# Performance work log

Measured on AMD Instinct MI355X. Metric: run time of the kernel, lower is better.

The kernel has to match this reference:

```python
import jax, jax.numpy as jnp
import numpy as np

N_NODES = 100000
N_EDGES = 3200000
NUM_GRAPHS = 128
IN_DIM = 15
HID = 64


def setup_inputs() -> dict:
    key = jax.random.key(0)
    ks = jax.random.split(key, 12)
    x = jax.random.normal(ks[0], (N_NODES, IN_DIM), dtype=jnp.float32)
    edge_index = jax.random.randint(ks[1], (2, N_EDGES), 0, N_NODES, dtype=jnp.int64)
    batch = jnp.sort(jax.random.randint(ks[2], (N_NODES,), 0, NUM_GRAPHS, dtype=jnp.int64))
    # Glorot-style weights for the 4 GCNConv layers, zero biases (PyG default)
    def glorot(k, fan_in, fan_out):
        s = jnp.sqrt(6.0 / (fan_in + fan_out))
        return jax.random.uniform(k, (fan_in, fan_out), jnp.float32, -s, s)
    return {
        "x": x,
        "w1": glorot(ks[3], IN_DIM, HID), "b1": jnp.zeros((HID,), jnp.float32),
        "w2": glorot(ks[4], HID, HID),    "b2": jnp.zeros((HID,), jnp.float32),
        "w3": glorot(ks[5], HID, HID),    "b3": jnp.zeros((HID,), jnp.float32),
        "w4": glorot(ks[6], HID, HID),    "b4": jnp.zeros((HID,), jnp.float32),
        "edge_index": edge_index,
        "batch": batch,
    }


def _gcn_norm(edge_index, num_nodes):
    # PyG gcn_norm with add_self_loops=True: A_hat = A + I, norm = d^-1/2[src] * d^-1/2[dst]
    loops = jnp.arange(num_nodes, dtype=edge_index.dtype)
    src = jnp.concatenate([edge_index[0], loops])
    dst = jnp.concatenate([edge_index[1], loops])
    deg = jax.ops.segment_sum(jnp.ones_like(dst, dtype=jnp.float32), dst,
                              num_segments=num_nodes)
    dis = jnp.where(deg > 0, jax.lax.rsqrt(deg), 0.0)
    norm = dis[src] * dis[dst]  # [E + N]
    return src, dst, norm


def _gcn_conv(h, w, b, src, dst, norm, num_nodes):
    h = h @ w                               # linear transform first (PyG order)
    msg = h[src] * norm[:, None]            # gather + scale  [E+N, HID]
    agg = jax.ops.segment_sum(msg, dst, num_segments=num_nodes)  # scatter-add
    return agg + b


def reference(x, w1, b1, w2, b2, w3, b3, w4, b4, edge_index, batch):
    n = x.shape[0]
    src, dst, norm = _gcn_norm(edge_index, n)
    h = jax.nn.relu(_gcn_conv(x, w1, b1, src, dst, norm, n))
    h = jax.nn.relu(_gcn_conv(h, w2, b2, src, dst, norm, n))
    h = jax.nn.relu(_gcn_conv(h, w3, b3, src, dst, norm, n))
    h = jax.nn.relu(_gcn_conv(h, w4, b4, src, dst, norm, n))
    # global_mean_pool over graph ids
    sums = jax.ops.segment_sum(h, batch, num_segments=NUM_GRAPHS)
    cnts = jax.ops.segment_sum(jnp.ones((n,), jnp.float32), batch,
                               num_segments=NUM_GRAPHS)
    return sums / jnp.maximum(cnts, 1.0)[:, None]
```

## Files before the change

kernel.cpp:

```cpp
#include <hip/hip_runtime.h>
#include <hip/hip_fp16.h>

#define NN 100000
#define NE 3200000
#define NG 128
#define HID 64

#define BSH 9
#define BNODES 512
#define NBK ((NN + BNODES - 1) / BNODES)
#define CCH 8192
#define CAP 18432

typedef __attribute__((ext_vector_type(2))) _Float16 half2v;
typedef __attribute__((ext_vector_type(4))) _Float16 half4v;

#if __has_builtin(__builtin_amdgcn_fdot2)
#define FDOT2(v, o, a) __builtin_amdgcn_fdot2((v), (o), (a), false)
#else
static __device__ inline float FDOT2(half2v v, half2v o, float a) {
    return a + (float)v.x * (float)o.x + (float)v.y * (float)o.y;
}
#endif

__global__ __launch_bounds__(256) void binit_kernel(int* __restrict__ bcur) {
    int t = threadIdx.x;
    if (t < NBK) bcur[t] = t * CAP;
}

__global__ __launch_bounds__(512) void bscatter_kernel(const int* __restrict__ src,
                                                       const int* __restrict__ dst,
                                                       int* __restrict__ bcur,
                                                       unsigned* __restrict__ pairs,
                                                       int E) {
    __shared__ unsigned stage[CCH];
    __shared__ unsigned char bb[CCH];
    __shared__ int cnt[NBK];
    __shared__ int base[NBK];
    const int e0 = blockIdx.x * CCH;
    const int n  = min(CCH, E - e0);
    if (n <= 0) return;
    for (int i = threadIdx.x; i < NBK; i += 512) cnt[i] = 0;
    __syncthreads();
    for (int i = threadIdx.x; i < n; i += 512) {
        int s = src[e0 + i], d = dst[e0 + i];
        int b = d >> BSH;
        stage[i] = ((unsigned)(d & (BNODES - 1)) << 17) | (unsigned)s;
        bb[i] = (unsigned char)b;
        atomicAdd(&cnt[b], 1);
    }
    __syncthreads();
    for (int i = threadIdx.x; i < NBK; i += 512) {
        int c = cnt[i];
        base[i] = c ? atomicAdd(&bcur[i], c) : 0;
        cnt[i] = 0;
    }
    __syncthreads();
    for (int i = threadIdx.x; i < n; i += 512) {
        int b = bb[i];
        int pos = base[b] + atomicAdd(&cnt[b], 1);
        if (pos < (b + 1) * CAP)
            pairs[pos] = stage[i];
    }
}

__global__ __launch_bounds__(512) void csr_kernel(const unsigned* __restrict__ pairs,
                                                  const int* __restrict__ bcur,
                                                  int2* __restrict__ rowse,
                                                  int* __restrict__ csr_src,
                                                  float* __restrict__ dis,
                                                  int N) {
    __shared__ unsigned stage[CAP];
    __shared__ int hist[BNODES];
    __shared__ int cur[BNODES];
    __shared__ int s[BNODES];
    const int b     = blockIdx.x;
    const int t     = threadIdx.x;
    const int node0 = b << BSH;
    const int nn    = min(BNODES, N - node0);
    const int p0    = b * CAP;
    const int cnt   = min(bcur[b] - p0, CAP);

    for (int i = t; i < cnt; i += 512) stage[i] = pairs[p0 + i];
    hist[t] = 0;
    __syncthreads();
    for (int i = t; i < cnt; i += 512)
        atomicAdd(&hist[stage[i] >> 17], 1);
    __syncthreads();

    int h = hist[t];
    s[t] = h;
    __syncthreads();
#pragma unroll
    for (int off = 1; off < BNODES; off <<= 1) {
        int u = (t >= off) ? s[t - off] : 0;
        __syncthreads();
        s[t] += u;
        __syncthreads();
    }
    int e0 = p0 + s[t] - h;
    if (t < nn) {
        rowse[node0 + t] = make_int2(e0, e0 + h);
        dis[node0 + t]   = rsqrtf((float)h + 1.0f);
    }
    cur[t] = e0;
    __syncthreads();

    for (int i = t; i < cnt; i += 512) {
        unsigned p = stage[i];
        int pos = atomicAdd(&cur[p >> 17], 1);
        csr_src[pos] = (int)(p & 0x1FFFFu);
    }
}

__global__ __launch_bounds__(256) void xprep_kernel(const float* __restrict__ x,
                                                    const float* __restrict__ dis,
                                                    __half* __restrict__ x16h, int N) {
    int gid = blockIdx.x * 256 + threadIdx.x;
    if (gid >= N * 16) return;
    int node = gid >> 4, k = gid & 15;
    float v = (k < 15) ? x[node * 15 + k] * dis[node] : 0.0f;
    x16h[gid] = __float2half(v);
}

__global__ __launch_bounds__(256) void gather16_kernel(const half4v* __restrict__ xh,
                                                       const int* __restrict__ csr_src,
                                                       const int2* __restrict__ rowse,
                                                       const float* __restrict__ dis,
                                                       float4* __restrict__ aggx, int N) {
    const int gid  = blockIdx.x * 256 + threadIdx.x;
    const int node = gid >> 2;
    if (node >= N) return;
    const int l  = threadIdx.x & 3;
    const int gb = threadIdx.x & 60;
    const int2 se = rowse[node];
    const int start = se.x, end = se.y;
    const half2v ONEX = {(_Float16)1.0f, (_Float16)0.0f};
    const half2v ONEY = {(_Float16)0.0f, (_Float16)1.0f};
    float a0 = 0.0f, a1 = 0.0f, a2 = 0.0f, a3 = 0.0f;
    for (int j0 = start; j0 < end; j0 += 4) {
        int j   = j0 + l;
        int s   = (j < end) ? csr_src[j] : 0;
        int cnt = min(4, end - j0);
#pragma unroll
        for (int k = 0; k < 4; ++k) {
            int sk = __shfl(s, gb + k);
            if (k < cnt) {
                half4v v = xh[sk * 4 + l];
                half2v p0 = __builtin_shufflevector(v, v, 0, 1);
                half2v p1 = __builtin_shufflevector(v, v, 2, 3);
                a0 = FDOT2(p0, ONEX, a0);
                a1 = FDOT2(p0, ONEY, a1);
                a2 = FDOT2(p1, ONEX, a2);
                a3 = FDOT2(p1, ONEY, a3);
            }
        }
    }
    half4v sv = xh[node * 4 + l];
    half2v s0 = __builtin_shufflevector(sv, sv, 0, 1);
    half2v s1 = __builtin_shufflevector(sv, sv, 2, 3);
    a0 += (float)s0.x; a1 += (float)s0.y;
    a2 += (float)s1.x; a3 += (float)s1.y;
    float sn = dis[node];
    aggx[(size_t)node * 4 + l] = make_float4(sn * a0, sn * a1, sn * a2, sn * a3);
}

__global__ __launch_bounds__(256) void gemm12_kernel(const float* __restrict__ in,
                                                     const float* __restrict__ w1,
                                                     const float* __restrict__ b1,
                                                     const float* __restrict__ w2,
                                                     const float* __restrict__ dis,
                                                     __half* __restrict__ th_out, int N) {
    __shared__ float w1_s[16 * 64];
    __shared__ float in_s[64 * 17];
    __shared__ float w2_s[64 * 64];
    __shared__ float h_s[64 * 65];
    const int tid  = threadIdx.x;
    const int row0 = blockIdx.x * 64;
    const int rows = min(64, N - row0);

    for (int i = tid; i < 16 * 64; i += 256) w1_s[i] = (i < 15 * 64) ? w1[i] : 0.0f;
    for (int i = tid; i < 64 * 64; i += 256) w2_s[i] = w2[i];
    for (int i = tid; i < rows * 16; i += 256) {
        int r = i >> 4, k = i & 15;
        in_s[r * 17 + k] = in[(size_t)(row0 + r) * 16 + k];
    }
    __syncthreads();

    const int r  = tid & 63;
    const int cg = tid >> 6;
    {
        float acc[16];
#pragma unroll
        for (int i = 0; i < 16; ++i) acc[i] = 0.0f;
#pragma unroll
        for (int k = 0; k < 16; ++k) {
            float a = in_s[r * 17 + k];
#pragma unroll
            for (int cc = 0; cc < 16; ++cc)
                acc[cc] += a * w1_s[k * 64 + cg * 16 + cc];
        }
#pragma unroll
        for (int cc = 0; cc < 16; ++cc)
            h_s[r * 65 + cg * 16 + cc] = fmaxf(acc[cc] + b1[cg * 16 + cc], 0.0f);
    }
    __syncthreads();
    {
        const float2* w2v = reinterpret_cast<const float2*>(w2_s);
        float2 acc2[8];
#pragma unroll
        for (int i = 0; i < 8; ++i) acc2[i] = make_float2(0.0f, 0.0f);
#pragma unroll
        for (int k = 0; k < 64; ++k) {
            float a = h_s[r * 65 + k];
            const float2* wk = w2v + k * 32 + cg * 8;
#pragma unroll
            for (int i = 0; i < 8; ++i) {
                float2 wv = wk[i];
                acc2[i].x += a * wv.x;
                acc2[i].y += a * wv.y;
            }
        }
        const int row = row0 + r;
        if (row < N) {
            float sd = dis[row];
            __align__(16) __half2 hh[8];
#pragma unroll
            for (int i = 0; i < 8; ++i)
                hh[i] = __floats2half2_rn(acc2[i].x * sd, acc2[i].y * sd);
            float4* tp = reinterpret_cast<float4*>(th_out + (size_t)row * HID + cg * 16);
            tp[0] = reinterpret_cast<float4*>(hh)[0];
            tp[1] = reinterpret_cast<float4*>(hh)[1];
        }
    }
}

__global__ __launch_bounds__(256) void fusedGG_kernel(const half2v* __restrict__ th_in,
                                                      const int* __restrict__ csr_src,
                                                      const int2* __restrict__ rowse,
                                                      const float* __restrict__ dis,
                                                      const float* __restrict__ w,
                                                      const float* __restrict__ bias,
                                                      __half* __restrict__ th_out, int N) {
    __shared__ float w_s[64 * 64];
    __shared__ float r_s[8][64];
    const int tid = threadIdx.x;
    {
        const float4* wsrc = reinterpret_cast<const float4*>(w);
        float4* wdst = reinterpret_cast<float4*>(w_s);
        for (int i = tid; i < 1024; i += 256) wdst[i] = wsrc[i];
    }
    const int g    = tid >> 5;
    const int node = blockIdx.x * 8 + g;
    const int l    = tid & 31;
    const int hb   = tid & 32;
    float u0 = 0.0f, u1 = 0.0f;
    if (node < N) {
        const int2 se = rowse[node];
        const int start = se.x, end = se.y;
        const half2v* tl = th_in + l;
        const half2v ONEX = {(_Float16)1.0f, (_Float16)0.0f};
        const half2v ONEY = {(_Float16)0.0f, (_Float16)1.0f};
        float ax = 0.0f, ay = 0.0f;
        for (int j0 = start; j0 < end; j0 += 32) {
            int j   = j0 + l;
            int s   = (j < end) ? csr_src[j] : 0;
            int cnt = min(32, end - j0);
            int k = 0;
            for (; k + 16 <= cnt; k += 16) {
                int sk[16];
#pragma unroll
                for (int u = 0; u < 16; ++u) sk[u] = __shfl(s, hb + k + u);
                half2v v[16];
#pragma unroll
                for (int u = 0; u < 16; ++u) v[u] = tl[sk[u] * 32];
#pragma unroll
                for (int u = 0; u < 16; ++u) {
                    ax = FDOT2(v[u], ONEX, ax);
                    ay = FDOT2(v[u], ONEY, ay);
                }
            }
            for (; k + 4 <= cnt; k += 4) {
                int s0 = __shfl(s, hb + k);
                int s1 = __shfl(s, hb + k + 1);
                int s2 = __shfl(s, hb + k + 2);
                int s3 = __shfl(s, hb + k + 3);
                half2v v0 = tl[s0 * 32];
                half2v v1 = tl[s1 * 32];
                half2v v2 = tl[s2 * 32];
                half2v v3 = tl[s3 * 32];
                ax = FDOT2(v0, ONEX, ax); ay = FDOT2(v0, ONEY, ay);
                ax = FDOT2(v1, ONEX, ax); ay = FDOT2(v1, ONEY, ay);
                ax = FDOT2(v2, ONEX, ax); ay = FDOT2(v2, ONEY, ay);
                ax = FDOT2(v3, ONEX, ax); ay = FDOT2(v3, ONEY, ay);
            }
            for (; k < cnt; ++k) {
                half2v v = tl[__shfl(s, hb + k) * 32];
                ax += (float)v.x; ay += (float)v.y;
            }
        }
        half2v self = tl[node * 32];
        ax += (float)self.x; ay += (float)self.y;
        float sn = dis[node];
        float2 bv = reinterpret_cast<const float2*>(bias)[l];
        u0 = fmaxf(sn * ax + bv.x, 0.0f);
        u1 = fmaxf(sn * ay + bv.y, 0.0f);
    }
    reinterpret_cast<float2*>(r_s[g])[l] = make_float2(u0, u1);
    __syncthreads();
    if (node < N) {
        const float2* wv = reinterpret_cast<const float2*>(w_s);
        float c0 = 0.0f, c1 = 0.0f;
#pragma unroll 8
        for (int k = 0; k < 64; ++k) {
            float u = r_s[g][k];
            float2 ww = wv[k * 32 + l];
            c0 += u * ww.x;
            c1 += u * ww.y;
        }
        float sd = dis[node];
        reinterpret_cast<__half2*>(th_out)[(size_t)node * 32 + l] =
            __floats2half2_rn(c0 * sd, c1 * sd);
    }
}

__global__ __launch_bounds__(256) void gatherh_pool_kernel(const half2v* __restrict__ th,
                                                           const int* __restrict__ csr_src,
                                                           const int2* __restrict__ rowse,
                                                           const float* __restrict__ dis,
                                                           const float* __restrict__ b4,
                                                           const int* __restrict__ batch,
                                                           float* __restrict__ sums,
                                                           float* __restrict__ cnts, int N) {
    __shared__ float lsum[4 * HID];
    __shared__ float lcnt[4];
    const int tid      = threadIdx.x;
    const int nodebase = blockIdx.x * 32;
    if (nodebase >= N) return;
    const int last   = min(nodebase + 32, N) - 1;
    const int gfirst = batch[nodebase];
    const int glast  = batch[last];
    const int span   = glast - gfirst + 1;

    for (int i = tid; i < 4 * HID; i += 256) lsum[i] = 0.0f;
    if (tid < 4) lcnt[tid] = 0.0f;
    __syncthreads();

    const int g  = tid >> 5;
    const int l  = tid & 31;
    const int hb = tid & 32;
    const half2v* tl = th + l;
    const half2v ONEX = {(_Float16)1.0f, (_Float16)0.0f};
    const half2v ONEY = {(_Float16)0.0f, (_Float16)1.0f};
    const float2 bv = reinterpret_cast<const float2*>(b4)[l];

    for (int it = 0; it < 4; ++it) {
        const int node = nodebase + it * 8 + g;
        if (node < N) {
            const int2 se = rowse[node];
            const int start = se.x, end = se.y;
            float ax = 0.0f, ay = 0.0f;
            for (int j0 = start; j0 < end; j0 += 32) {
                int j   = j0 + l;
                int s   = (j < end) ? csr_src[j] : 0;
                int cnt = min(32, end - j0);
                int k = 0;
                for (; k + 16 <= cnt; k += 16) {
                    int sk[16];
#pragma unroll
                    for (int u = 0; u < 16; ++u) sk[u] = __shfl(s, hb + k + u);
                    half2v v[16];
#pragma unroll
                    for (int u = 0; u < 16; ++u) v[u] = tl[sk[u] * 32];
#pragma unroll
                    for (int u = 0; u < 16; ++u) {
                        ax = FDOT2(v[u], ONEX, ax);
                        ay = FDOT2(v[u], ONEY, ay);
                    }
                }
                for (; k + 4 <= cnt; k += 4) {
                    int s0 = __shfl(s, hb + k);
                    int s1 = __shfl(s, hb + k + 1);
                    int s2 = __shfl(s, hb + k + 2);
                    int s3 = __shfl(s, hb + k + 3);
                    half2v v0 = tl[s0 * 32];
                    half2v v1 = tl[s1 * 32];
                    half2v v2 = tl[s2 * 32];
                    half2v v3 = tl[s3 * 32];
                    ax = FDOT2(v0, ONEX, ax); ay = FDOT2(v0, ONEY, ay);
                    ax = FDOT2(v1, ONEX, ax); ay = FDOT2(v1, ONEY, ay);
                    ax = FDOT2(v2, ONEX, ax); ay = FDOT2(v2, ONEY, ay);
                    ax = FDOT2(v3, ONEX, ax); ay = FDOT2(v3, ONEY, ay);
                }
                for (; k < cnt; ++k) {
                    half2v v = tl[__shfl(s, hb + k) * 32];
                    ax += (float)v.x; ay += (float)v.y;
                }
            }
            half2v self = tl[node * 32];
            ax += (float)self.x; ay += (float)self.y;
            const float sn = dis[node];
            const float v0 = fmaxf(fmaf(sn, ax, bv.x), 0.0f);
            const float v1 = fmaxf(fmaf(sn, ay, bv.y), 0.0f);
            const int slot = batch[node] - gfirst;
            if (slot < 4) {
                atomicAdd(&lsum[slot * HID + 2 * l], v0);
                atomicAdd(&lsum[slot * HID + 2 * l + 1], v1);
                if (l == 0) atomicAdd(&lcnt[slot], 1.0f);
            } else {
                atomicAdd(&sums[(size_t)(gfirst + slot) * HID + 2 * l], v0);
                atomicAdd(&sums[(size_t)(gfirst + slot) * HID + 2 * l + 1], v1);
                if (l == 0) atomicAdd(&cnts[gfirst + slot], 1.0f);
            }
        }
    }
    __syncthreads();

    const int flush = min(span, 4) * HID;
    for (int i = tid; i < flush; i += 256)
        if (lsum[i] != 0.0f) atomicAdd(&sums[(size_t)gfirst * HID + i], lsum[i]);
    if (tid < 4 && tid < span && lcnt[tid] != 0.0f)
        atomicAdd(&cnts[gfirst + tid], lcnt[tid]);
}

__global__ __launch_bounds__(256) void finalize_kernel(const float* __restrict__ sums,
                                                       const float* __restrict__ cnts,
                                                       float* __restrict__ out) {
    int i = blockIdx.x * 256 + threadIdx.x;
    if (i < NG * HID) out[i] = sums[i] / fmaxf(cnts[i >> 6], 1.0f);
}

extern "C" void kernel_launch(void* const* d_in, const int* in_sizes, int n_in,
                              void* d_out, int out_size, void* d_ws, size_t ws_size,
                              hipStream_t stream) {
    const float* x  = (const float*)d_in[0];
    const float* w1 = (const float*)d_in[1];
    const float* b1 = (const float*)d_in[2];
    const float* w2 = (const float*)d_in[3];
    const float* b2 = (const float*)d_in[4];
    const float* w3 = (const float*)d_in[5];
    const float* b3 = (const float*)d_in[6];
    const float* w4 = (const float*)d_in[7];
    const float* b4 = (const float*)d_in[8];
    const int* ei    = (const int*)d_in[9];
    const int* batch = (const int*)d_in[10];
    const int* src = ei;
    const int* dst = ei + NE;

    __half*   thB      = (__half*)d_ws;
    __half*   thA      = thB + (size_t)NN * HID;
    unsigned* pairs    = (unsigned*)(thA + (size_t)NN * HID);
    __half*   x16h     = (__half*)pairs;
    float*    aggx     = (float*)(x16h + (size_t)NN * 16);
    int*      csr_src  = (int*)(pairs + (size_t)NBK * CAP);
    int2*     rowse    = (int2*)(csr_src + (size_t)NBK * CAP);
    float*    dis      = (float*)(rowse + NN);
    int*      bcur     = (int*)(dis + NN);
    float*    sums     = (float*)(bcur + NBK);
    float*    cnts     = sums + NG * HID;

    float* out = (float*)d_out;

    const int GB  = (NN + 63) / 64;
    const int XB  = (NN * 16 + 255) / 256;
    const int OB  = (NN * 4 + 255) / 256;
    const int FB  = (NN + 7) / 8;
    const int PB  = (NN + 31) / 32;
    const int CB  = (NE + CCH - 1) / CCH;

    hipMemsetAsync(sums, 0, (NG * HID + NG) * sizeof(float), stream);

    binit_kernel<<<1, 256, 0, stream>>>(bcur);
    bscatter_kernel<<<CB, 512, 0, stream>>>(src, dst, bcur, pairs, NE);
    csr_kernel<<<NBK, 512, 0, stream>>>(pairs, bcur, rowse, csr_src, dis, NN);

    xprep_kernel<<<XB, 256, 0, stream>>>(x, dis, x16h, NN);
    gather16_kernel<<<OB, 256, 0, stream>>>((const half4v*)x16h, csr_src, rowse,
                                            dis, (float4*)aggx, NN);
    gemm12_kernel<<<GB, 256, 0, stream>>>(aggx, w1, b1, w2, dis, thA, NN);
    fusedGG_kernel<<<FB, 256, 0, stream>>>((const half2v*)thA, csr_src, rowse,
                                           dis, w3, b2, thB, NN);
    fusedGG_kernel<<<FB, 256, 0, stream>>>((const half2v*)thB, csr_src, rowse,
                                           dis, w4, b3, thA, NN);
    gatherh_pool_kernel<<<PB, 256, 0, stream>>>((const half2v*)thA, csr_src, rowse,
                                                dis, b4, batch, sums, cnts, NN);

    finalize_kernel<<<(NG * HID + 255) / 256, 256, 0, stream>>>(sums, cnts, out);
}
```

Measured before the change: 441.4 us.

## Sort edges by bucket in shared memory before coalesced writes; shrink pool blocks

The bucket scatter kernel now does a block-level prefix scan over per-bucket counts, reorders staged edges into bucket-contiguous order in shared memory, and then writes them so consecutive threads store to consecutive global addresses. The previous version wrote each edge to a scattered position. The edge chunk per block is halved so the extra shared arrays fit. The pooling kernel processes 16 nodes per block instead of 32, launching more blocks with shorter per-block work. The trade-off is extra synchronisation, a serial per-bucket fill loop, and more atomics on the global bucket cursors.

```diff
diff --git a/kernel.cpp b/kernel.cpp
--- a/kernel.cpp
+++ b/kernel.cpp
@@ -9,7 +9,7 @@
 #define BSH 9
 #define BNODES 512
 #define NBK ((NN + BNODES - 1) / BNODES)
-#define CCH 8192
+#define CCH 4096
 #define CAP 18432
 
 typedef __attribute__((ext_vector_type(2))) _Float16 half2v;
@@ -34,15 +34,21 @@
                                                        unsigned* __restrict__ pairs,
                                                        int E) {
     __shared__ unsigned stage[CCH];
+    __shared__ unsigned ordered[CCH];
     __shared__ unsigned char bb[CCH];
+    __shared__ unsigned char bucket_of[CCH];
     __shared__ int cnt[NBK];
-    __shared__ int base[NBK];
+    __shared__ int cur[NBK];
+    __shared__ int lbase[NBK];
+    __shared__ int gbase[NBK];
+    __shared__ int sc[256];
     const int e0 = blockIdx.x * CCH;
     const int n  = min(CCH, E - e0);
     if (n <= 0) return;
-    for (int i = threadIdx.x; i < NBK; i += 512) cnt[i] = 0;
-    __syncthreads();
-    for (int i = threadIdx.x; i < n; i += 512) {
+    const int t = threadIdx.x;
+    for (int i = t; i < NBK; i += 512) cnt[i] = 0;
+    __syncthreads();
+    for (int i = t; i < n; i += 512) {
         int s = src[e0 + i], d = dst[e0 + i];
         int b = d >> BSH;
         stage[i] = ((unsigned)(d & (BNODES - 1)) << 17) | (unsigned)s;
@@ -50,17 +56,33 @@
         atomicAdd(&cnt[b], 1);
     }
     __syncthreads();
-    for (int i = threadIdx.x; i < NBK; i += 512) {
-        int c = cnt[i];
-        base[i] = c ? atomicAdd(&bcur[i], c) : 0;
-        cnt[i] = 0;
-    }
-    __syncthreads();
-    for (int i = threadIdx.x; i < n; i += 512) {
-        int b = bb[i];
-        int pos = base[b] + atomicAdd(&cnt[b], 1);
+    if (t < 256) sc[t] = (t < NBK) ? cnt[t] : 0;
+    __syncthreads();
+    for (int off = 1; off < 256; off <<= 1) {
+        int u = (t < 256 && t >= off) ? sc[t - off] : 0;
+        __syncthreads();
+        if (t < 256) sc[t] += u;
+        __syncthreads();
+    }
+    if (t < NBK) {
+        int c  = cnt[t];
+        int lb = sc[t] - c;
+        lbase[t] = lb;
+        cur[t]   = lb;
+        gbase[t] = c ? atomicAdd(&bcur[t], c) : 0;
+        for (int j = 0; j < c; ++j) bucket_of[lb + j] = (unsigned char)t;
+    }
+    __syncthreads();
+    for (int i = t; i < n; i += 512) {
+        int p = atomicAdd(&cur[bb[i]], 1);
+        ordered[p] = stage[i];
+    }
+    __syncthreads();
+    for (int j = t; j < n; j += 512) {
+        int b   = bucket_of[j];
+        int pos = gbase[b] + (j - lbase[b]);
         if (pos < (b + 1) * CAP)
-            pairs[pos] = stage[i];
+            pairs[pos] = ordered[j];
     }
 }
 
@@ -335,9 +357,9 @@
     __shared__ float lsum[4 * HID];
     __shared__ float lcnt[4];
     const int tid      = threadIdx.x;
-    const int nodebase = blockIdx.x * 32;
+    const int nodebase = blockIdx.x * 16;
     if (nodebase >= N) return;
-    const int last   = min(nodebase + 32, N) - 1;
+    const int last   = min(nodebase + 16, N) - 1;
     const int gfirst = batch[nodebase];
     const int glast  = batch[last];
     const int span   = glast - gfirst + 1;
@@ -354,7 +376,7 @@
     const half2v ONEY = {(_Float16)0.0f, (_Float16)1.0f};
     const float2 bv = reinterpret_cast<const float2*>(b4)[l];
 
-    for (int it = 0; it < 4; ++it) {
+    for (int it = 0; it < 2; ++it) {
         const int node = nodebase + it * 8 + g;
         if (node < N) {
             const int2 se = rowse[node];
@@ -465,7 +487,7 @@
     const int XB  = (NN * 16 + 255) / 256;
     const int OB  = (NN * 4 + 255) / 256;
     const int FB  = (NN + 7) / 8;
-    const int PB  = (NN + 31) / 32;
+    const int PB  = (NN + 15) / 16;
     const int CB  = (NE + CCH - 1) / CCH;
 
     hipMemsetAsync(sums, 0, (NG * HID + NG) * sizeof(float), stream);
```

After: 453.9 us. 1.03x slower.

## Fuse x prep into CSR build and layer-1 gather into GEMM kernel

Applied to the files above, without the earlier changes.

Removes the bucket-init kernel by zeroing bucket counters with the existing memset and adding the bucket base offset inside the scatter. The x scaling and fp16 conversion move into the tail of the CSR kernel, reusing the degree it has just computed. The 16-wide neighbour gather is merged into the first GEMM kernel, so aggregated features go to shared memory instead of a global round trip. This saves three launches and the aggx traffic, at the cost of more work per block in the fused kernels.

```diff
diff --git a/kernel.cpp b/kernel.cpp
--- a/kernel.cpp
+++ b/kernel.cpp
@@ -22,11 +22,6 @@
     return a + (float)v.x * (float)o.x + (float)v.y * (float)o.y;
 }
 #endif
-
-__global__ __launch_bounds__(256) void binit_kernel(int* __restrict__ bcur) {
-    int t = threadIdx.x;
-    if (t < NBK) bcur[t] = t * CAP;
-}
 
 __global__ __launch_bounds__(512) void bscatter_kernel(const int* __restrict__ src,
                                                        const int* __restrict__ dst,
@@ -52,7 +47,7 @@
     __syncthreads();
     for (int i = threadIdx.x; i < NBK; i += 512) {
         int c = cnt[i];
-        base[i] = c ? atomicAdd(&bcur[i], c) : 0;
+        base[i] = c ? (i * CAP + atomicAdd(&bcur[i], c)) : 0;
         cnt[i] = 0;
     }
     __syncthreads();
@@ -66,9 +61,11 @@
 
 __global__ __launch_bounds__(512) void csr_kernel(const unsigned* __restrict__ pairs,
                                                   const int* __restrict__ bcur,
+                                                  const float* __restrict__ x,
                                                   int2* __restrict__ rowse,
                                                   int* __restrict__ csr_src,
                                                   float* __restrict__ dis,
+                                                  __half* __restrict__ x16h,
                                                   int N) {
     __shared__ unsigned stage[CAP];
     __shared__ int hist[BNODES];
@@ -79,7 +76,7 @@
     const int node0 = b << BSH;
     const int nn    = min(BNODES, N - node0);
     const int p0    = b * CAP;
-    const int cnt   = min(bcur[b] - p0, CAP);
+    const int cnt   = min(bcur[b], CAP);
 
     for (int i = t; i < cnt; i += 512) stage[i] = pairs[p0 + i];
     hist[t] = 0;
@@ -99,9 +96,10 @@
         __syncthreads();
     }
     int e0 = p0 + s[t] - h;
+    float sn = rsqrtf((float)h + 1.0f);
     if (t < nn) {
         rowse[node0 + t] = make_int2(e0, e0 + h);
-        dis[node0 + t]   = rsqrtf((float)h + 1.0f);
+        dis[node0 + t]   = sn;
     }
     cur[t] = e0;
     __syncthreads();
@@ -111,79 +109,77 @@
         int pos = atomicAdd(&cur[p >> 17], 1);
         csr_src[pos] = (int)(p & 0x1FFFFu);
     }
-}
-
-__global__ __launch_bounds__(256) void xprep_kernel(const float* __restrict__ x,
-                                                    const float* __restrict__ dis,
-                                                    __half* __restrict__ x16h, int N) {
-    int gid = blockIdx.x * 256 + threadIdx.x;
-    if (gid >= N * 16) return;
-    int node = gid >> 4, k = gid & 15;
-    float v = (k < 15) ? x[node * 15 + k] * dis[node] : 0.0f;
-    x16h[gid] = __float2half(v);
-}
-
-__global__ __launch_bounds__(256) void gather16_kernel(const half4v* __restrict__ xh,
-                                                       const int* __restrict__ csr_src,
-                                                       const int2* __restrict__ rowse,
-                                                       const float* __restrict__ dis,
-                                                       float4* __restrict__ aggx, int N) {
-    const int gid  = blockIdx.x * 256 + threadIdx.x;
-    const int node = gid >> 2;
-    if (node >= N) return;
-    const int l  = threadIdx.x & 3;
-    const int gb = threadIdx.x & 60;
-    const int2 se = rowse[node];
-    const int start = se.x, end = se.y;
-    const half2v ONEX = {(_Float16)1.0f, (_Float16)0.0f};
-    const half2v ONEY = {(_Float16)0.0f, (_Float16)1.0f};
-    float a0 = 0.0f, a1 = 0.0f, a2 = 0.0f, a3 = 0.0f;
-    for (int j0 = start; j0 < end; j0 += 4) {
-        int j   = j0 + l;
-        int s   = (j < end) ? csr_src[j] : 0;
-        int cnt = min(4, end - j0);
-#pragma unroll
-        for (int k = 0; k < 4; ++k) {
-            int sk = __shfl(s, gb + k);
-            if (k < cnt) {
-                half4v v = xh[sk * 4 + l];
-                half2v p0 = __builtin_shufflevector(v, v, 0, 1);
-                half2v p1 = __builtin_shufflevector(v, v, 2, 3);
-                a0 = FDOT2(p0, ONEX, a0);
-                a1 = FDOT2(p0, ONEY, a1);
-                a2 = FDOT2(p1, ONEX, a2);
-                a3 = FDOT2(p1, ONEY, a3);
-            }
-        }
-    }
-    half4v sv = xh[node * 4 + l];
-    half2v s0 = __builtin_shufflevector(sv, sv, 0, 1);
-    half2v s1 = __builtin_shufflevector(sv, sv, 2, 3);
-    a0 += (float)s0.x; a1 += (float)s0.y;
-    a2 += (float)s1.x; a3 += (float)s1.y;
-    float sn = dis[node];
-    aggx[(size_t)node * 4 + l] = make_float4(sn * a0, sn * a1, sn * a2, sn * a3);
-}
-
-__global__ __launch_bounds__(256) void gemm12_kernel(const float* __restrict__ in,
-                                                     const float* __restrict__ w1,
-                                                     const float* __restrict__ b1,
-                                                     const float* __restrict__ w2,
-                                                     const float* __restrict__ dis,
-                                                     __half* __restrict__ th_out, int N) {
+
+    if (t < nn) {
+        const int node = node0 + t;
+        const float* xp = x + (size_t)node * 15;
+        __align__(16) __half xr[16];
+#pragma unroll
+        for (int j = 0; j < 15; ++j) xr[j] = __float2half(xp[j] * sn);
+        xr[15] = __float2half(0.0f);
+        float4* dst4 = reinterpret_cast<float4*>(x16h + (size_t)node * 16);
+        dst4[0] = reinterpret_cast<const float4*>(xr)[0];
+        dst4[1] = reinterpret_cast<const float4*>(xr)[1];
+    }
+}
+
+__global__ __launch_bounds__(256) void gg12_kernel(const half4v* __restrict__ xh,
+                                                   const int* __restrict__ csr_src,
+                                                   const int2* __restrict__ rowse,
+                                                   const float* __restrict__ dis,
+                                                   const float* __restrict__ w1,
+                                                   const float* __restrict__ b1,
+                                                   const float* __restrict__ w2,
+                                                   __half* __restrict__ th_out, int N) {
     __shared__ float w1_s[16 * 64];
+    __shared__ float w2_s[64 * 64];
     __shared__ float in_s[64 * 17];
-    __shared__ float w2_s[64 * 64];
     __shared__ float h_s[64 * 65];
     const int tid  = threadIdx.x;
     const int row0 = blockIdx.x * 64;
-    const int rows = min(64, N - row0);
 
     for (int i = tid; i < 16 * 64; i += 256) w1_s[i] = (i < 15 * 64) ? w1[i] : 0.0f;
     for (int i = tid; i < 64 * 64; i += 256) w2_s[i] = w2[i];
-    for (int i = tid; i < rows * 16; i += 256) {
-        int r = i >> 4, k = i & 15;
-        in_s[r * 17 + k] = in[(size_t)(row0 + r) * 16 + k];
+
+    {
+        const int r    = tid >> 2;
+        const int node = row0 + r;
+        const int l    = tid & 3;
+        const int gb   = tid & 60;
+        const half2v ONEX = {(_Float16)1.0f, (_Float16)0.0f};
+        const half2v ONEY = {(_Float16)0.0f, (_Float16)1.0f};
+        float a0 = 0.0f, a1 = 0.0f, a2 = 0.0f, a3 = 0.0f;
+        if (node < N) {
+            const int2 se = rowse[node];
+            const int start = se.x, end = se.y;
+            for (int j0 = start; j0 < end; j0 += 4) {
+                int j   = j0 + l;
+                int sidx = (j < end) ? csr_src[j] : 0;
+                int cnt = min(4, end - j0);
+#pragma unroll
+                for (int k = 0; k < 4; ++k) {
+                    int sk = __shfl(sidx, gb + k);
+                    if (k < cnt) {
+                        half4v v = xh[sk * 4 + l];
+                        half2v p0 = __builtin_shufflevector(v, v, 0, 1);
+                        half2v p1 = __builtin_shufflevector(v, v, 2, 3);
+                        a0 = FDOT2(p0, ONEX, a0);
+                        a1 = FDOT2(p0, ONEY, a1);
+                        a2 = FDOT2(p1, ONEX, a2);
+                        a3 = FDOT2(p1, ONEY, a3);
+                    }
+                }
+            }
+            half4v sv = xh[node * 4 + l];
+            half2v s0 = __builtin_shufflevector(sv, sv, 0, 1);
+            half2v s1 = __builtin_shufflevector(sv, sv, 2, 3);
+            a0 += (float)s0.x; a1 += (float)s0.y;
+            a2 += (float)s1.x; a3 += (float)s1.y;
+            float sn = dis[node];
+            a0 *= sn; a1 *= sn; a2 *= sn; a3 *= sn;
+        }
+        float* ip = in_s + r * 17 + 4 * l;
+        ip[0] = a0; ip[1] = a1; ip[2] = a2; ip[3] = a3;
     }
     __syncthreads();
 
@@ -450,34 +446,28 @@
     __half*   thB      = (__half*)d_ws;
     __half*   thA      = thB + (size_t)NN * HID;
     unsigned* pairs    = (unsigned*)(thA + (size_t)NN * HID);
-    __half*   x16h     = (__half*)pairs;
-    float*    aggx     = (float*)(x16h + (size_t)NN * 16);
     int*      csr_src  = (int*)(pairs + (size_t)NBK * CAP);
     int2*     rowse    = (int2*)(csr_src + (size_t)NBK * CAP);
     float*    dis      = (float*)(rowse + NN);
     int*      bcur     = (int*)(dis + NN);
     float*    sums     = (float*)(bcur + NBK);
     float*    cnts     = sums + NG * HID;
+    __half*   x16h     = (__half*)(cnts + NG);
 
     float* out = (float*)d_out;
 
     const int GB  = (NN + 63) / 64;
-    const int XB  = (NN * 16 + 255) / 256;
-    const int OB  = (NN * 4 + 255) / 256;
     const int FB  = (NN + 7) / 8;
     const int PB  = (NN + 31) / 32;
     const int CB  = (NE + CCH - 1) / CCH;
 
-    hipMemsetAsync(sums, 0, (NG * HID + NG) * sizeof(float), stream);
-
-    binit_kernel<<<1, 256, 0, stream>>>(bcur);
+    hipMemsetAsync(bcur, 0, (NBK + NG * HID + NG) * sizeof(int), stream);
+
     bscatter_kernel<<<CB, 512, 0, stream>>>(src, dst, bcur, pairs, NE);
-    csr_kernel<<<NBK, 512, 0, stream>>>(pairs, bcur, rowse, csr_src, dis, NN);
-
-    xprep_kernel<<<XB, 256, 0, stream>>>(x, dis, x16h, NN);
-    gather16_kernel<<<OB, 256, 0, stream>>>((const half4v*)x16h, csr_src, rowse,
-                                            dis, (float4*)aggx, NN);
-    gemm12_kernel<<<GB, 256, 0, stream>>>(aggx, w1, b1, w2, dis, thA, NN);
+    csr_kernel<<<NBK, 512, 0, stream>>>(pairs, bcur, x, rowse, csr_src, dis, x16h, NN);
+
+    gg12_kernel<<<GB, 256, 0, stream>>>((const half4v*)x16h, csr_src, rowse, dis,
+                                        w1, b1, w2, thA, NN);
     fusedGG_kernel<<<FB, 256, 0, stream>>>((const half2v*)thA, csr_src, rowse,
                                            dis, w3, b2, thB, NN);
     fusedGG_kernel<<<FB, 256, 0, stream>>>((const half2v*)thB, csr_src, rowse,
```

After: 459.5 us. 1.04x slower.
